# Kernel tuning notes

Measured on AMD Instinct MI355X. Metric: run time of the kernel, lower is better.

## Reference

```python
import jax, jax.numpy as jnp
import numpy as np

N = 100000      # nodes
E = 1600000     # edges
D_IN = 2        # num_node_features (hardcoded in module)
EMB = 64        # embedding_size
HID = 128       # hidden_size
NEG_SLOPE = 0.2 # GATv2 leaky_relu default


def setup_inputs() -> dict:
    key = jax.random.key(0)
    ks = jax.random.split(key, 20)
    s = 0.1
    inp = {
        "x": jax.random.normal(ks[0], (N, D_IN), dtype=jnp.float32),
        "edge_index": jax.random.randint(ks[1], (2, E), 0, N, dtype=jnp.int32),
        "edge_attr": jax.random.normal(ks[2], (E, 1), dtype=jnp.float32),
        "target_node_idx": 12345,
        # conv1 params (in=2 -> out=64, heads=1)
        "Wl1": jax.random.normal(ks[3], (D_IN, EMB), dtype=jnp.float32) * s,
        "bl1": jnp.zeros((EMB,), dtype=jnp.float32),
        "Wr1": jax.random.normal(ks[4], (D_IN, EMB), dtype=jnp.float32) * s,
        "br1": jnp.zeros((EMB,), dtype=jnp.float32),
        "We1": jax.random.normal(ks[5], (1, EMB), dtype=jnp.float32) * s,
        "att1": jax.random.normal(ks[6], (EMB,), dtype=jnp.float32) * s,
        "b1": jnp.zeros((EMB,), dtype=jnp.float32),
        # conv2 params (in=64 -> out=64)
        "Wl2": jax.random.normal(ks[7], (EMB, EMB), dtype=jnp.float32) * s,
        "bl2": jnp.zeros((EMB,), dtype=jnp.float32),
        "Wr2": jax.random.normal(ks[8], (EMB, EMB), dtype=jnp.float32) * s,
        "br2": jnp.zeros((EMB,), dtype=jnp.float32),
        "We2": jax.random.normal(ks[9], (1, EMB), dtype=jnp.float32) * s,
        "att2": jax.random.normal(ks[10], (EMB,), dtype=jnp.float32) * s,
        "b2": jnp.zeros((EMB,), dtype=jnp.float32),
        # final linear head
        "Wf": jax.random.normal(ks[11], (EMB, HID), dtype=jnp.float32) * s,
        "bf": jnp.zeros((HID,), dtype=jnp.float32),
    }
    return inp


def _gatv2_layer(x, src, dst, ea, Wl, bl, Wr, br, We, att, b):
    # GATv2: e_ij = att . leaky_relu(Wl x_j + Wr x_i + We ea_ij); out_i = sum_j softmax_i(e_ij) * (Wl x_j)
    xl = x @ Wl + bl                      # [N, C] (source transform)
    xr = x @ Wr + br                      # [N, C] (target transform)
    ee = ea @ We                          # [E', C]
    e = jax.nn.leaky_relu(xl[src] + xr[dst] + ee, NEG_SLOPE)  # [E', C]
    score = e @ att                       # [E']
    m = jax.ops.segment_max(score, dst, num_segments=N)
    ex = jnp.exp(score - m[dst])
    denom = jax.ops.segment_sum(ex, dst, num_segments=N)
    alpha = ex / denom[dst]               # segment softmax over incoming edges
    out = jax.ops.segment_sum(alpha[:, None] * xl[src], dst, num_segments=N)
    return out + b


def reference(x, edge_index, edge_attr, target_node_idx,
              Wl1, bl1, Wr1, br1, We1, att1, b1,
              Wl2, bl2, Wr2, br2, We2, att2, b2,
              Wf, bf):
    # PyG add_self_loops=True with fill_value='mean' for edge_attr
    loop = jnp.arange(N, dtype=edge_index.dtype)
    src = jnp.concatenate([edge_index[0], loop])
    dst = jnp.concatenate([edge_index[1], loop])
    ea_mean = jnp.mean(edge_attr, axis=0, keepdims=True)          # [1,1]
    ea = jnp.concatenate([edge_attr, jnp.broadcast_to(ea_mean, (N, 1))])

    h = _gatv2_layer(x, src, dst, ea, Wl1, bl1, Wr1, br1, We1, att1, b1)
    h = jax.nn.relu(h)
    h = _gatv2_layer(h, src, dst, ea, Wl2, bl2, Wr2, br2, We2, att2, b2)
    h = jax.nn.relu(h)

    t = h[target_node_idx][None, :]       # [1, EMB]
    return t @ Wf + bf                    # [1, HID]
```

## Files before the change

kernel.cpp:

```cpp
#include <hip/hip_runtime.h>
#include <math.h>

#define CAP2   511
#define CAPS1  512
#define CAPN   512
#define NBLK   896
#define NLEAF  64
#define BMW    4096


__device__ __forceinline__ int aload_i(const int* p) {
    return __hip_atomic_load((int*)p, __ATOMIC_RELAXED, __HIP_MEMORY_SCOPE_AGENT);
}
__device__ __forceinline__ void astore_i(int* p, int v) {
    __hip_atomic_store(p, v, __ATOMIC_RELAXED, __HIP_MEMORY_SCOPE_AGENT);
}
__device__ __forceinline__ float aload_f(const float* p) {
    return __hip_atomic_load((float*)p, __ATOMIC_RELAXED, __HIP_MEMORY_SCOPE_AGENT);
}
__device__ __forceinline__ void astore_f(float* p, float v) {
    __hip_atomic_store(p, v, __ATOMIC_RELAXED, __HIP_MEMORY_SCOPE_AGENT);
}
__device__ __forceinline__ unsigned long long aload_u64(const unsigned long long* p) {
    return __hip_atomic_load((unsigned long long*)p, __ATOMIC_RELAXED, __HIP_MEMORY_SCOPE_AGENT);
}
__device__ __forceinline__ void astore_u64(unsigned long long* p, unsigned long long v) {
    __hip_atomic_store(p, v, __ATOMIC_RELAXED, __HIP_MEMORY_SCOPE_AGENT);
}

__device__ __forceinline__ void grid_sync(int* bar, int epoch) {
    __syncthreads();
    if (threadIdx.x < 64) {
        int lane = threadIdx.x;
        if (lane == 0)
            __hip_atomic_fetch_add(&bar[32 * (blockIdx.x & (NLEAF - 1))], 1,
                                   __ATOMIC_RELAXED, __HIP_MEMORY_SCOPE_AGENT);
        if (blockIdx.x == 0) {
            int target = (epoch + 1) * NBLK;
            for (;;) {
                int v = __hip_atomic_load(&bar[32 * lane], __ATOMIC_RELAXED,
                                          __HIP_MEMORY_SCOPE_AGENT);
                for (int o = 32; o >= 1; o >>= 1) v += __shfl_xor(v, o, 64);
                if (v >= target) break;
                __builtin_amdgcn_s_sleep(1);
            }
            if (lane == 0)
                __hip_atomic_store(&bar[32 * NLEAF], epoch + 1,
                                   __ATOMIC_RELAXED, __HIP_MEMORY_SCOPE_AGENT);
        } else if (lane == 0) {
            while (__hip_atomic_load(&bar[32 * NLEAF], __ATOMIC_RELAXED,
                                     __HIP_MEMORY_SCOPE_AGENT) < epoch + 1)
                __builtin_amdgcn_s_sleep(2);
        }
    }
    __syncthreads();
}

__global__ __launch_bounds__(256, 4)
void k_mega(const float* __restrict__ x, const int* __restrict__ ei,
            const float* __restrict__ ea, const int* __restrict__ tptr,
            const float* __restrict__ Wl1, const float* __restrict__ bl1,
            const float* __restrict__ Wr1, const float* __restrict__ br1,
            const float* __restrict__ We1, const float* __restrict__ att1,
            const float* __restrict__ b1,
            const float* __restrict__ Wl2, const float* __restrict__ bl2,
            const float* __restrict__ Wr2, const float* __restrict__ br2,
            const float* __restrict__ We2, const float* __restrict__ att2,
            const float* __restrict__ b2,
            const float* __restrict__ Wf, const float* __restrict__ bf,
            int E,
            int* hdr, int* bar, int* nodecnt, float* partials,
            int* L2_src, float* L2_ea,
            unsigned long long* buck,
            float* xl2, float* out) {
    int tid = threadIdx.x, lane = tid & 63, wq = tid >> 6;
    int bid = blockIdx.x;
    int gid = bid * 256 + tid;
    const int gstride = NBLK * 256;

    __shared__ float wsum[4];
    __shared__ int   s1[CAPS1];
    __shared__ int   l2idx[CAP2];
    __shared__ int   esrc[CAPN + 1];
    __shared__ float eea[CAPN + 1];
    __shared__ float xsA[CAPN + 1], xsB[CAPN + 1];
    __shared__ float scores[CAPN + 1];
    __shared__ float part[4][64];
    __shared__ float hrow[64];
    __shared__ float xr2s[64];
    __shared__ int   bitmap[BMW];
    __shared__ float m_sh, d_sh, eam_sh;
    __shared__ int   n_sh;

    const int4*   dst4 = (const int4*)(ei + E);
    const float4* ea4  = (const float4*)ea;
    int E4 = E >> 2;
    int t = tptr[0];

    {
        float local = 0.f;
        for (int e4 = gid; e4 < E4; e4 += gstride) {
            int4 d = dst4[e4];
            float4 a = ea4[e4];
            local += a.x + a.y + a.z + a.w;
            int eb = e4 * 4;
            if (d.x == t) { int p = atomicAdd(&hdr[0], 1); if (p < CAP2) { astore_i(&L2_src[p], ei[eb]);     astore_f(&L2_ea[p], a.x); } }
            if (d.y == t) { int p = atomicAdd(&hdr[0], 1); if (p < CAP2) { astore_i(&L2_src[p], ei[eb + 1]); astore_f(&L2_ea[p], a.y); } }
            if (d.z == t) { int p = atomicAdd(&hdr[0], 1); if (p < CAP2) { astore_i(&L2_src[p], ei[eb + 2]); astore_f(&L2_ea[p], a.z); } }
            if (d.w == t) { int p = atomicAdd(&hdr[0], 1); if (p < CAP2) { astore_i(&L2_src[p], ei[eb + 3]); astore_f(&L2_ea[p], a.w); } }
        }
        if (gid == 0) {
            for (int e = E4 * 4; e < E; e++) {
                float a = ea[e];
                local += a;
                if (ei[E + e] == t) { int p = atomicAdd(&hdr[0], 1); if (p < CAP2) { astore_i(&L2_src[p], ei[e]); astore_f(&L2_ea[p], a); } }
            }
        }
        for (int o = 32; o >= 1; o >>= 1) local += __shfl_xor(local, o, 64);
        if (lane == 0) wsum[wq] = local;
        __syncthreads();
        if (tid == 0) astore_f(&partials[bid], wsum[0] + wsum[1] + wsum[2] + wsum[3]);
    }
    grid_sync(bar, 0);

    int c2 = aload_i(&hdr[0]); if (c2 > CAP2) c2 = CAP2;
    {
        float local = 0.f;
        for (int k = tid; k < NBLK; k += 256) local += aload_f(&partials[k]);
        for (int o = 32; o >= 1; o >>= 1) local += __shfl_xor(local, o, 64);
        if (lane == 0) wsum[wq] = local;
        __syncthreads();
        if (tid == 0) eam_sh = (wsum[0] + wsum[1] + wsum[2] + wsum[3]) / (float)E;

        if (wq == 0) {
            if (c2 <= 64) {
                int v = (lane < c2) ? aload_i(&L2_src[lane]) : -1;
                int first = lane;
                #pragma unroll
                for (int j = 0; j < 64; j++) {
                    int vj = __shfl(v, j);
                    if (j < first && vj == v) first = j;
                }
                bool isfirst = (lane < c2) && (first == lane) && (v != t);
                unsigned long long bfm = __ballot(isfirst);
                int myidx = (v == t) ? 0
                            : (1 + (int)__popcll(bfm & ((1ull << lane) - 1)));
                int idx = __shfl(myidx, first);
                if (lane < c2) l2idx[lane] = idx;
                if (isfirst) s1[myidx] = v;
                if (lane == 0) { s1[0] = t; n_sh = 1 + (int)__popcll(bfm); }
            } else if (lane == 0) {
                s1[0] = t;
                int n = 1;
                for (int k = 0; k < c2; k++) {
                    int v = aload_i(&L2_src[k]);
                    int idx = -1;
                    for (int j = 0; j < n; j++) if (s1[j] == v) { idx = j; break; }
                    if (idx < 0) { idx = n; s1[n] = v; n++; }
                    l2idx[k] = idx;
                }
                n_sh = n;
            }
        }
        for (int w = tid; w < BMW; w += 256) bitmap[w] = 0;
        __syncthreads();
        int n_s1 = n_sh;
        for (int j = tid; j < n_s1; j += 256) {
            int u = s1[j];
            atomicOr(&bitmap[(u >> 5) & (BMW - 1)], 1 << (u & 31));
        }
        __syncthreads();

        for (int e4 = gid; e4 < E4; e4 += gstride) {
            int4 d = dst4[e4];
            int eb = e4 * 4;
            int dd[4] = {d.x, d.y, d.z, d.w};
            #pragma unroll
            for (int q = 0; q < 4; q++) {
                int dv = dd[q];
                if (bitmap[(dv >> 5) & (BMW - 1)] & (1 << (dv & 31))) {
                    int idx = -1;
                    for (int j = 0; j < n_s1; j++) if (s1[j] == dv) { idx = j; break; }
                    if (idx >= 0) {
                        int slot = __hip_atomic_fetch_add(&nodecnt[idx], 1,
                                     __ATOMIC_RELAXED, __HIP_MEMORY_SCOPE_AGENT);
                        if (slot < CAPN) {
                            unsigned long long pk =
                                ((unsigned long long)__float_as_uint(ea[eb + q]) << 32) |
                                (unsigned)ei[eb + q];
                            astore_u64(&buck[(size_t)idx * CAPN + slot], pk);
                        }
                    }
                }
            }
        }
        if (gid == 0) {
            for (int e = E4 * 4; e < E; e++) {
                int dv = ei[E + e];
                int idx = -1;
                for (int j = 0; j < n_s1; j++) if (s1[j] == dv) { idx = j; break; }
                if (idx >= 0) {
                    int slot = __hip_atomic_fetch_add(&nodecnt[idx], 1,
                                 __ATOMIC_RELAXED, __HIP_MEMORY_SCOPE_AGENT);
                    if (slot < CAPN) {
                        unsigned long long pk =
                            ((unsigned long long)__float_as_uint(ea[e]) << 32) |
                            (unsigned)ei[e];
                        astore_u64(&buck[(size_t)idx * CAPN + slot], pk);
                    }
                }
            }
        }
    }
    grid_sync(bar, 1);

    int n_s1 = n_sh;
    float eam = eam_sh;

    for (int node = bid; node < n_s1; node += NBLK) {
        int v = s1[node];
        int cnt = aload_i(&nodecnt[node]); if (cnt > CAPN) cnt = CAPN;
        for (int k = tid; k < cnt; k += 256) {
            unsigned long long pk = aload_u64(&buck[(size_t)node * CAPN + k]);
            esrc[k] = (int)(unsigned)(pk & 0xffffffffull);
            eea[k]  = __uint_as_float((unsigned)(pk >> 32));
        }
        __syncthreads();
        int nE = cnt;
        if (tid == 0) { esrc[nE] = v; eea[nE] = eam; }
        __syncthreads();
        nE += 1;

        const float2* x2 = (const float2*)x;
        for (int j = tid; j < nE; j += 256) {
            float2 xv = x2[esrc[j]];
            xsA[j] = xv.x; xsB[j] = xv.y;
        }
        __syncthreads();

        float wl0 = Wl1[lane], wl1w = Wl1[64 + lane], bl = bl1[lane];
        float we = We1[lane], at = att1[lane];
        float2 xv = x2[v];
        float xr = xv.x * Wr1[lane] + xv.y * Wr1[64 + lane] + br1[lane];

        for (int k = wq; k < nE; k += 4) {
            float xl = xsA[k] * wl0 + xsB[k] * wl1w + bl;
            float ev = xl + xr + eea[k] * we;
            ev = ev > 0.f ? ev : 0.2f * ev;
            float p = ev * at;
            for (int o = 32; o >= 1; o >>= 1) p += __shfl_xor(p, o, 64);
            if (lane == 0) scores[k] = p;
        }
        __syncthreads();

        if (wq == 0) {
            float m = -3.4e38f;
            for (int k = lane; k < nE; k += 64) m = fmaxf(m, scores[k]);
            for (int o = 32; o >= 1; o >>= 1) m = fmaxf(m, __shfl_xor(m, o, 64));
            float d = 0.f;
            for (int k = lane; k < nE; k += 64) d += expf(scores[k] - m);
            for (int o = 32; o >= 1; o >>= 1) d += __shfl_xor(d, o, 64);
            if (lane == 0) { m_sh = m; d_sh = d; }
        }
        __syncthreads();
        float m = m_sh, dinv = 1.f / d_sh;

        float acc = 0.f;
        for (int k = wq; k < nE; k += 4) {
            float xl = xsA[k] * wl0 + xsB[k] * wl1w + bl;
            acc += expf(scores[k] - m) * dinv * xl;
        }
        part[wq][lane] = acc;
        __syncthreads();
        if (tid < 64) {
            float h = part[0][lane] + part[1][lane] + part[2][lane] + part[3][lane] + b1[lane];
            hrow[lane] = h > 0.f ? h : 0.f;
        }
        __syncthreads();

        float p = 0.f;
        int k0 = 16 * wq;
        for (int k = k0; k < k0 + 16; k++) p += hrow[k] * Wl2[k * 64 + lane];
        part[wq][lane] = p;
        __syncthreads();
        if (tid < 64)
            astore_f(&xl2[node * 64 + lane],
                     part[0][lane] + part[1][lane] + part[2][lane] + part[3][lane] + bl2[lane]);

        if (node == 0) {
            __syncthreads();
            float p2 = 0.f;
            for (int k = k0; k < k0 + 16; k++) p2 += hrow[k] * Wr2[k * 64 + lane];
            part[wq][lane] = p2;
            __syncthreads();
            if (tid < 64)
                xr2s[lane] = part[0][lane] + part[1][lane] + part[2][lane] + part[3][lane] + br2[lane];
        }
        __syncthreads();
    }
    grid_sync(bar, 2);

    if (bid == 0) {
        int nE2 = c2;
        float* xl2sh = (float*)bitmap;
        int rows = n_s1 < 64 ? n_s1 : 64;
        for (int i = tid; i < rows * 64; i += 256) xl2sh[i] = aload_f(&xl2[i]);
        for (int j = tid; j < nE2; j += 256) eea[j] = aload_f(&L2_ea[j]);
        __syncthreads();

        float we = We2[lane], at = att2[lane], xr = xr2s[lane];
        for (int j = wq; j <= nE2; j += 4) {
            int   idx = (j < nE2) ? l2idx[j] : 0;
            float eav = (j < nE2) ? eea[j]   : eam;
            float xlv = (idx < 64) ? xl2sh[idx * 64 + lane]
                                   : aload_f(&xl2[idx * 64 + lane]);
            float ev = xlv + xr + eav * we;
            ev = ev > 0.f ? ev : 0.2f * ev;
            float p = ev * at;
            for (int o = 32; o >= 1; o >>= 1) p += __shfl_xor(p, o, 64);
            if (lane == 0) scores[j] = p;
        }
        __syncthreads();

        if (wq == 0) {
            int tot = nE2 + 1;
            float m = -3.4e38f;
            for (int j = lane; j < tot; j += 64) m = fmaxf(m, scores[j]);
            for (int o = 32; o >= 1; o >>= 1) m = fmaxf(m, __shfl_xor(m, o, 64));
            float d = 0.f;
            for (int j = lane; j < tot; j += 64) d += expf(scores[j] - m);
            for (int o = 32; o >= 1; o >>= 1) d += __shfl_xor(d, o, 64);
            if (lane == 0) { m_sh = m; d_sh = d; }
        }
        __syncthreads();
        float m = m_sh, dinv = 1.f / d_sh;

        float acc = 0.f;
        for (int j = wq; j <= nE2; j += 4) {
            int idx = (j < nE2) ? l2idx[j] : 0;
            float xlv = (idx < 64) ? xl2sh[idx * 64 + lane]
                                   : aload_f(&xl2[idx * 64 + lane]);
            acc += expf(scores[j] - m) * dinv * xlv;
        }
        part[wq][lane] = acc;
        __syncthreads();
        if (tid < 64) {
            float h = part[0][lane] + part[1][lane] + part[2][lane] + part[3][lane] + b2[lane];
            hrow[lane] = h > 0.f ? h : 0.f;
        }
        __syncthreads();
        if (tid < 128) {
            float r = bf[tid];
            for (int c = 0; c < 64; c++) r += hrow[c] * Wf[c * 128 + tid];
            out[tid] = r;
        }
    }
}

extern "C" void kernel_launch(void* const* d_in, const int* in_sizes, int n_in,
                              void* d_out, int out_size, void* d_ws, size_t ws_size,
                              hipStream_t stream) {
    const float* x    = (const float*)d_in[0];
    const int*   ei   = (const int*)  d_in[1];
    const float* ea   = (const float*)d_in[2];
    const int*   tptr = (const int*)  d_in[3];
    const float* Wl1  = (const float*)d_in[4];
    const float* bl1  = (const float*)d_in[5];
    const float* Wr1  = (const float*)d_in[6];
    const float* br1  = (const float*)d_in[7];
    const float* We1  = (const float*)d_in[8];
    const float* att1 = (const float*)d_in[9];
    const float* b1   = (const float*)d_in[10];
    const float* Wl2  = (const float*)d_in[11];
    const float* bl2  = (const float*)d_in[12];
    const float* Wr2  = (const float*)d_in[13];
    const float* br2  = (const float*)d_in[14];
    const float* We2  = (const float*)d_in[15];
    const float* att2 = (const float*)d_in[16];
    const float* b2   = (const float*)d_in[17];
    const float* Wf   = (const float*)d_in[18];
    const float* bf   = (const float*)d_in[19];

    int E = in_sizes[2];

    char* base = (char*)d_ws;
    int*   hdr      = (int*)base;   base += 256;
    int*   bar      = (int*)base;   base += 8448;
    int*   nodecnt  = (int*)base;   base += 2048;
    float* partials = (float*)base; base += NBLK * sizeof(float);
    int*   L2_src   = (int*)base;   base += 512 * sizeof(int);
    float* L2_ea    = (float*)base; base += 512 * sizeof(float);
    unsigned long long* buck = (unsigned long long*)base;
    base += (size_t)CAPS1 * CAPN * sizeof(unsigned long long);
    float* xl2      = (float*)base; base += (size_t)CAPS1 * 64 * sizeof(float);

    hipMemsetAsync(hdr, 0, 256 + 8448 + 2048, stream);

    hipLaunchKernelGGL(k_mega, dim3(NBLK), dim3(256), 0, stream,
                       x, ei, ea, tptr,
                       Wl1, bl1, Wr1, br1, We1, att1, b1,
                       Wl2, bl2, Wr2, br2, We2, att2, b2,
                       Wf, bf, E,
                       hdr, bar, nodecnt, partials,
                       L2_src, L2_ea,
                       buck, xl2, (float*)d_out);
}
```

Baseline: 132.2 us.

## Split megakernel into a wide edge-scan kernel and a small 64-block kernel

The first edge pass, which gathers the target's incoming edges and sums the edge attributes, moves into its own kernel with 2048 blocks. A kernel boundary now replaces the first software grid barrier. The rest runs in a 64-block kernel, where a flat grid barrier replaces the 896-block tree barrier, so synchronisation should be cheaper. The risk is that the second full-edge scan, which finds edges into the neighbour set, now runs on only 64 blocks and may become latency or bandwidth bound.

```diff
diff --git a/kernel.cpp b/kernel.cpp
--- a/kernel.cpp
+++ b/kernel.cpp
@@ -4,17 +4,14 @@
 #define CAP2   511
 #define CAPS1  512
 #define CAPN   512
-#define NBLK   896
-#define NLEAF  64
+#define NBLK1  2048
+#define MBLK   64
 #define BMW    4096
 
 
 __device__ __forceinline__ int aload_i(const int* p) {
     return __hip_atomic_load((int*)p, __ATOMIC_RELAXED, __HIP_MEMORY_SCOPE_AGENT);
 }
-__device__ __forceinline__ void astore_i(int* p, int v) {
-    __hip_atomic_store(p, v, __ATOMIC_RELAXED, __HIP_MEMORY_SCOPE_AGENT);
-}
 __device__ __forceinline__ float aload_f(const float* p) {
     return __hip_atomic_load((float*)p, __ATOMIC_RELAXED, __HIP_MEMORY_SCOPE_AGENT);
 }
@@ -28,55 +25,88 @@
     __hip_atomic_store(p, v, __ATOMIC_RELAXED, __HIP_MEMORY_SCOPE_AGENT);
 }
 
-__device__ __forceinline__ void grid_sync(int* bar, int epoch) {
+__device__ __forceinline__ void grid_sync64(int* bar, int epoch) {
     __syncthreads();
-    if (threadIdx.x < 64) {
+    if (threadIdx.x == 0)
+        __hip_atomic_fetch_add(&bar[32 * blockIdx.x], 1,
+                               __ATOMIC_RELAXED, __HIP_MEMORY_SCOPE_AGENT);
+    if (blockIdx.x == 0 && threadIdx.x < 64) {
         int lane = threadIdx.x;
+        int target = (epoch + 1) * MBLK;
+        for (;;) {
+            int v = __hip_atomic_load(&bar[32 * lane], __ATOMIC_RELAXED,
+                                      __HIP_MEMORY_SCOPE_AGENT);
+            for (int o = 32; o >= 1; o >>= 1) v += __shfl_xor(v, o, 64);
+            if (v >= target) break;
+            __builtin_amdgcn_s_sleep(1);
+        }
         if (lane == 0)
-            __hip_atomic_fetch_add(&bar[32 * (blockIdx.x & (NLEAF - 1))], 1,
-                                   __ATOMIC_RELAXED, __HIP_MEMORY_SCOPE_AGENT);
-        if (blockIdx.x == 0) {
-            int target = (epoch + 1) * NBLK;
-            for (;;) {
-                int v = __hip_atomic_load(&bar[32 * lane], __ATOMIC_RELAXED,
-                                          __HIP_MEMORY_SCOPE_AGENT);
-                for (int o = 32; o >= 1; o >>= 1) v += __shfl_xor(v, o, 64);
-                if (v >= target) break;
-                __builtin_amdgcn_s_sleep(1);
-            }
-            if (lane == 0)
-                __hip_atomic_store(&bar[32 * NLEAF], epoch + 1,
-                                   __ATOMIC_RELAXED, __HIP_MEMORY_SCOPE_AGENT);
-        } else if (lane == 0) {
-            while (__hip_atomic_load(&bar[32 * NLEAF], __ATOMIC_RELAXED,
-                                     __HIP_MEMORY_SCOPE_AGENT) < epoch + 1)
-                __builtin_amdgcn_s_sleep(2);
-        }
+            __hip_atomic_store(&bar[32 * MBLK], epoch + 1,
+                               __ATOMIC_RELAXED, __HIP_MEMORY_SCOPE_AGENT);
+    } else if (threadIdx.x == 0) {
+        while (__hip_atomic_load(&bar[32 * MBLK], __ATOMIC_RELAXED,
+                                 __HIP_MEMORY_SCOPE_AGENT) < epoch + 1)
+            __builtin_amdgcn_s_sleep(2);
     }
     __syncthreads();
 }
 
-__global__ __launch_bounds__(256, 4)
-void k_mega(const float* __restrict__ x, const int* __restrict__ ei,
-            const float* __restrict__ ea, const int* __restrict__ tptr,
-            const float* __restrict__ Wl1, const float* __restrict__ bl1,
-            const float* __restrict__ Wr1, const float* __restrict__ br1,
-            const float* __restrict__ We1, const float* __restrict__ att1,
-            const float* __restrict__ b1,
-            const float* __restrict__ Wl2, const float* __restrict__ bl2,
-            const float* __restrict__ Wr2, const float* __restrict__ br2,
-            const float* __restrict__ We2, const float* __restrict__ att2,
-            const float* __restrict__ b2,
-            const float* __restrict__ Wf, const float* __restrict__ bf,
-            int E,
-            int* hdr, int* bar, int* nodecnt, float* partials,
-            int* L2_src, float* L2_ea,
-            unsigned long long* buck,
-            float* xl2, float* out) {
+__global__ __launch_bounds__(256)
+void k_scan1(const int* __restrict__ ei, const float* __restrict__ ea,
+             const int* __restrict__ tptr, int E,
+             int* hdr, int* L2_src, float* L2_ea, float* partials) {
+    int tid = threadIdx.x, lane = tid & 63, wq = tid >> 6;
+    int gid = blockIdx.x * 256 + tid;
+    int t = tptr[0];
+    int E4 = E >> 2;
+    float local = 0.f;
+    __shared__ float wsum[4];
+
+    for (int e4 = gid; e4 < E4; e4 += NBLK1 * 256) {
+        int4   d = ((const int4*)(ei + E))[e4];
+        float4 a = ((const float4*)ea)[e4];
+        local += a.x + a.y + a.z + a.w;
+        int eb = e4 * 4;
+        if (d.x == t) { int p = atomicAdd(&hdr[0], 1); if (p < CAP2) { L2_src[p] = ei[eb];     L2_ea[p] = a.x; } }
+        if (d.y == t) { int p = atomicAdd(&hdr[0], 1); if (p < CAP2) { L2_src[p] = ei[eb + 1]; L2_ea[p] = a.y; } }
+        if (d.z == t) { int p = atomicAdd(&hdr[0], 1); if (p < CAP2) { L2_src[p] = ei[eb + 2]; L2_ea[p] = a.z; } }
+        if (d.w == t) { int p = atomicAdd(&hdr[0], 1); if (p < CAP2) { L2_src[p] = ei[eb + 3]; L2_ea[p] = a.w; } }
+    }
+    if (gid == 0) {
+        for (int e = E4 * 4; e < E; e++) {
+            float a = ea[e];
+            local += a;
+            if (ei[E + e] == t) { int p = atomicAdd(&hdr[0], 1); if (p < CAP2) { L2_src[p] = ei[e]; L2_ea[p] = a; } }
+        }
+    }
+    for (int o = 32; o >= 1; o >>= 1) local += __shfl_xor(local, o, 64);
+    if (lane == 0) wsum[wq] = local;
+    __syncthreads();
+    if (tid == 0) partials[blockIdx.x] = wsum[0] + wsum[1] + wsum[2] + wsum[3];
+}
+
+__global__ __launch_bounds__(256)
+void k_mid(const float* __restrict__ x, const int* __restrict__ ei,
+           const float* __restrict__ ea, const int* __restrict__ tptr,
+           const float* __restrict__ Wl1, const float* __restrict__ bl1,
+           const float* __restrict__ Wr1, const float* __restrict__ br1,
+           const float* __restrict__ We1, const float* __restrict__ att1,
+           const float* __restrict__ b1,
+           const float* __restrict__ Wl2, const float* __restrict__ bl2,
+           const float* __restrict__ Wr2, const float* __restrict__ br2,
+           const float* __restrict__ We2, const float* __restrict__ att2,
+           const float* __restrict__ b2,
+           const float* __restrict__ Wf, const float* __restrict__ bf,
+           int E,
+           const int* __restrict__ hdr, int* bar, int* nodecnt,
+           const float* __restrict__ partials,
+           const int* __restrict__ L2_src, const float* __restrict__ L2_ea,
+           unsigned long long* buck, float* xl2, float* out) {
     int tid = threadIdx.x, lane = tid & 63, wq = tid >> 6;
     int bid = blockIdx.x;
     int gid = bid * 256 + tid;
-    const int gstride = NBLK * 256;
+    int t = tptr[0];
+    int E4 = E >> 2;
 
     __shared__ float wsum[4];
     __shared__ int   s1[CAPS1];
@@ -92,49 +122,18 @@
     __shared__ float m_sh, d_sh, eam_sh;
     __shared__ int   n_sh;
 
-    const int4*   dst4 = (const int4*)(ei + E);
-    const float4* ea4  = (const float4*)ea;
-    int E4 = E >> 2;
-    int t = tptr[0];
-
+    int c2 = hdr[0]; if (c2 > CAP2) c2 = CAP2;
     {
         float local = 0.f;
-        for (int e4 = gid; e4 < E4; e4 += gstride) {
-            int4 d = dst4[e4];
-            float4 a = ea4[e4];
-            local += a.x + a.y + a.z + a.w;
-            int eb = e4 * 4;
-            if (d.x == t) { int p = atomicAdd(&hdr[0], 1); if (p < CAP2) { astore_i(&L2_src[p], ei[eb]);     astore_f(&L2_ea[p], a.x); } }
-            if (d.y == t) { int p = atomicAdd(&hdr[0], 1); if (p < CAP2) { astore_i(&L2_src[p], ei[eb + 1]); astore_f(&L2_ea[p], a.y); } }
-            if (d.z == t) { int p = atomicAdd(&hdr[0], 1); if (p < CAP2) { astore_i(&L2_src[p], ei[eb + 2]); astore_f(&L2_ea[p], a.z); } }
-            if (d.w == t) { int p = atomicAdd(&hdr[0], 1); if (p < CAP2) { astore_i(&L2_src[p], ei[eb + 3]); astore_f(&L2_ea[p], a.w); } }
-        }
-        if (gid == 0) {
-            for (int e = E4 * 4; e < E; e++) {
-                float a = ea[e];
-                local += a;
-                if (ei[E + e] == t) { int p = atomicAdd(&hdr[0], 1); if (p < CAP2) { astore_i(&L2_src[p], ei[e]); astore_f(&L2_ea[p], a); } }
-            }
-        }
+        for (int k = tid; k < NBLK1; k += 256) local += partials[k];
         for (int o = 32; o >= 1; o >>= 1) local += __shfl_xor(local, o, 64);
         if (lane == 0) wsum[wq] = local;
         __syncthreads();
-        if (tid == 0) astore_f(&partials[bid], wsum[0] + wsum[1] + wsum[2] + wsum[3]);
-    }
-    grid_sync(bar, 0);
-
-    int c2 = aload_i(&hdr[0]); if (c2 > CAP2) c2 = CAP2;
-    {
-        float local = 0.f;
-        for (int k = tid; k < NBLK; k += 256) local += aload_f(&partials[k]);
-        for (int o = 32; o >= 1; o >>= 1) local += __shfl_xor(local, o, 64);
-        if (lane == 0) wsum[wq] = local;
-        __syncthreads();
         if (tid == 0) eam_sh = (wsum[0] + wsum[1] + wsum[2] + wsum[3]) / (float)E;
 
         if (wq == 0) {
             if (c2 <= 64) {
-                int v = (lane < c2) ? aload_i(&L2_src[lane]) : -1;
+                int v = (lane < c2) ? L2_src[lane] : -1;
                 int first = lane;
                 #pragma unroll
                 for (int j = 0; j < 64; j++) {
@@ -153,7 +152,7 @@
                 s1[0] = t;
                 int n = 1;
                 for (int k = 0; k < c2; k++) {
-                    int v = aload_i(&L2_src[k]);
+                    int v = L2_src[k];
                     int idx = -1;
                     for (int j = 0; j < n; j++) if (s1[j] == v) { idx = j; break; }
                     if (idx < 0) { idx = n; s1[n] = v; n++; }
@@ -171,8 +170,8 @@
         }
         __syncthreads();
 
-        for (int e4 = gid; e4 < E4; e4 += gstride) {
-            int4 d = dst4[e4];
+        for (int e4 = gid; e4 < E4; e4 += MBLK * 256) {
+            int4 d = ((const int4*)(ei + E))[e4];
             int eb = e4 * 4;
             int dd[4] = {d.x, d.y, d.z, d.w};
             #pragma unroll
@@ -212,12 +211,12 @@
             }
         }
     }
-    grid_sync(bar, 1);
+    grid_sync64(bar, 0);
 
     int n_s1 = n_sh;
     float eam = eam_sh;
 
-    for (int node = bid; node < n_s1; node += NBLK) {
+    for (int node = bid; node < n_s1; node += MBLK) {
         int v = s1[node];
         int cnt = aload_i(&nodecnt[node]); if (cnt > CAPN) cnt = CAPN;
         for (int k = tid; k < cnt; k += 256) {
@@ -298,14 +297,14 @@
         }
         __syncthreads();
     }
-    grid_sync(bar, 2);
+    grid_sync64(bar, 1);
 
     if (bid == 0) {
         int nE2 = c2;
         float* xl2sh = (float*)bitmap;
         int rows = n_s1 < 64 ? n_s1 : 64;
         for (int i = tid; i < rows * 64; i += 256) xl2sh[i] = aload_f(&xl2[i]);
-        for (int j = tid; j < nE2; j += 256) eea[j] = aload_f(&L2_ea[j]);
+        for (int j = tid; j < nE2; j += 256) eea[j] = L2_ea[j];
         __syncthreads();
 
         float we = We2[lane], at = att2[lane], xr = xr2s[lane];
@@ -387,7 +386,7 @@
     int*   hdr      = (int*)base;   base += 256;
     int*   bar      = (int*)base;   base += 8448;
     int*   nodecnt  = (int*)base;   base += 2048;
-    float* partials = (float*)base; base += NBLK * sizeof(float);
+    float* partials = (float*)base; base += NBLK1 * sizeof(float);
     int*   L2_src   = (int*)base;   base += 512 * sizeof(int);
     float* L2_ea    = (float*)base; base += 512 * sizeof(float);
     unsigned long long* buck = (unsigned long long*)base;
@@ -396,12 +395,13 @@
 
     hipMemsetAsync(hdr, 0, 256 + 8448 + 2048, stream);
 
-    hipLaunchKernelGGL(k_mega, dim3(NBLK), dim3(256), 0, stream,
+    hipLaunchKernelGGL(k_scan1, dim3(NBLK1), dim3(256), 0, stream,
+                       ei, ea, tptr, E, hdr, L2_src, L2_ea, partials);
+    hipLaunchKernelGGL(k_mid, dim3(MBLK), dim3(256), 0, stream,
                        x, ei, ea, tptr,
                        Wl1, bl1, Wr1, br1, We1, att1, b1,
                        Wl2, bl2, Wr2, br2, We2, att2, b2,
                        Wf, bf, E,
                        hdr, bar, nodecnt, partials,
-                       L2_src, L2_ea,
-                       buck, xl2, (float*)d_out);
-}
+                       L2_src, L2_ea, buck, xl2, (float*)d_out);
+}
```

Result: slower. 140.4 us (+6.2%).
